# Kernel tuning notes

Measured on AMD Instinct MI355X. Metric: run time of the kernel, lower is better.

The kernel has to match this reference:

```python
import jax, jax.numpy as jnp
import numpy as np

B, S, E, HD = 32, 1024, 768, 64


def _rope_tables(seq_len, dim):
    # theta = 10000 ** (-2*arange(0,dim,2)/dim); freqs = pos * theta
    theta = jnp.power(10000.0, -2.0 * jnp.arange(0, dim, 2, dtype=jnp.float32) / dim)
    pos = jnp.arange(seq_len, dtype=jnp.float32)[:, None]          # [S,1]
    freqs = pos * theta[None, :]                                    # [S,dim//2]
    cos = jnp.repeat(jnp.cos(freqs), 2, axis=-1)                    # [S,dim]
    sin = jnp.repeat(jnp.sin(freqs), 2, axis=-1)                    # [S,dim]
    return cos, sin


def _apply_rope(x, cos, sin):
    # rotate-half interleaved: new[...,0::2] = -x[...,1::2]; new[...,1::2] = x[...,0::2]
    b, s, d = x.shape
    x2 = x.reshape(b, s, d // 2, 2)
    rot = jnp.stack([-x2[..., 1], x2[..., 0]], axis=-1).reshape(b, s, d)
    return x * cos[None] + rot * sin[None]


def setup_inputs() -> dict:
    key = jax.random.key(0)
    k0, k1, k2, k3 = jax.random.split(key, 4)
    x = jax.random.normal(k0, (B, S, E), dtype=jnp.float32)
    Wq = jax.random.normal(k1, (HD, E), dtype=jnp.float32) * 0.02
    Wk = jax.random.normal(k2, (HD, E), dtype=jnp.float32) * 0.02
    Wv = jax.random.normal(k3, (HD, E), dtype=jnp.float32) * 0.02
    return {"x": x, "Wq": Wq, "Wk": Wk, "Wv": Wv}


def reference(x, Wq, Wk, Wv):
    b, s, e = x.shape
    q = jnp.einsum('bse,he->bsh', x, Wq)
    k = jnp.einsum('bse,he->bsh', x, Wk)
    v = jnp.einsum('bse,he->bsh', x, Wv)
    cos, sin = _rope_tables(s, q.shape[-1])
    rq = _apply_rope(q, cos, sin)
    rk = _apply_rope(k, cos, sin)
    scale = e ** (-0.5)  # NOTE: original scales by emb_dim, not head_size
    scores = jnp.einsum('bqh,bkh->bqk', rq, rk) * scale
    causal = jnp.tril(jnp.ones((s, s), dtype=bool))
    scores = jnp.where(causal[None], scores, -jnp.inf)
    attn = jax.nn.softmax(scores, axis=-1)
    return jnp.einsum('bqk,bkh->bqh', attn, v)
```

## Files before the change

kernel.cpp:

```cpp
#include <hip/hip_runtime.h>
#include <hip/hip_bf16.h>

#define B_  32
#define S_  1024
#define E_  768
#define HD_ 64
#define M_  (B_*S_)

typedef __attribute__((ext_vector_type(8))) short short8;
typedef __attribute__((ext_vector_type(4))) float float4v;

__device__ __forceinline__ unsigned short f2bf(float x) {
    union { float f; unsigned u; } c; c.f = x;
    unsigned r = (c.u + 0x7FFFu + ((c.u >> 16) & 1u)) >> 16;
    return (unsigned short)r;
}

__device__ __forceinline__ void gld_lds16(const void* g, void* l) {
    __builtin_amdgcn_global_load_lds(
        (const __attribute__((address_space(1))) unsigned int*)g,
        (__attribute__((address_space(3))) unsigned int*)l,
        16, 0, 0);
}

__global__ __launch_bounds__(256) void setup_kernel(const unsigned int* __restrict__ xw,
                                                    unsigned int* __restrict__ flag,
                                                    float* __restrict__ cs_t,
                                                    float* __restrict__ sn_t) {
    if (blockIdx.x == 128) {
        __shared__ int cnt;
        if (threadIdx.x == 0) cnt = 0;
        __syncthreads();
        unsigned int w = xw[(size_t)threadIdx.x * 33331];
        unsigned int e = (w >> 8) & 0x7F;
        int hit = (e >= 0x3B && e <= 0x40) ? 1 : 0;
        atomicAdd(&cnt, hit);
        __syncthreads();
        if (threadIdx.x == 0) *flag = (cnt > 128) ? 1u : 0u;
        return;
    }
    int idx = blockIdx.x * 256 + threadIdx.x;
    int pos = idx >> 5;
    int ii  = idx & 31;
    float theta = exp2f(-(float)ii * 0.8304820237218406f);
    float fr = (float)pos * theta;
    float sn, cs;
    sincosf(fr, &sn, &cs);
    cs_t[idx] = cs;
    sn_t[idx] = sn;
}

__global__ __launch_bounds__(256) void wpack_kernel(
    const void* __restrict__ Wq_, const void* __restrict__ Wk_,
    const void* __restrict__ Wv_, const unsigned int* __restrict__ flag,
    unsigned short* __restrict__ wp)
{
    const bool isb = (*flag != 0);
    int gid  = blockIdx.x * 256 + threadIdx.x;
    int lane = gid & 63;
    int tIdx = gid >> 6;
    int ct   = tIdx / 24;
    int rem  = tIdx - ct * 24;
    int c    = rem >> 1, ks = rem & 1;
    int quad = lane >> 4, l15 = lane & 15;
    const void* wsel = (ct < 4) ? Wq_ : (ct < 8 ? Wk_ : Wv_);
    int row = (ct & 3) * 16 + l15;
    int col = c * 64 + ks * 32 + quad * 8;
    uint4 w;
    if (isb) {
        w = *(const uint4*)((const unsigned short*)wsel + (size_t)row * E_ + col);
    } else {
        const float* f = (const float*)wsel + (size_t)row * E_ + col;
        float4 a = *(const float4*)f, bq = *(const float4*)(f + 4);
        w.x = f2bf(a.x)  | ((unsigned)f2bf(a.y)  << 16);
        w.y = f2bf(a.z)  | ((unsigned)f2bf(a.w)  << 16);
        w.z = f2bf(bq.x) | ((unsigned)f2bf(bq.y) << 16);
        w.w = f2bf(bq.z) | ((unsigned)f2bf(bq.w) << 16);
    }
    *(uint4*)(wp + (size_t)gid * 8) = w;
}

__global__ __launch_bounds__(512, 2) void qkv_mfma_kernel(
    const void* __restrict__ x_, const unsigned short* __restrict__ wp,
    const unsigned int* __restrict__ flag,
    const float* __restrict__ cs_t, const float* __restrict__ sn_t,
    unsigned short* __restrict__ rq_p, unsigned short* __restrict__ rk_p,
    unsigned short* __restrict__ vt_p)
{
    __shared__ __align__(16) unsigned short Alds[64 * 768];
    __shared__ __align__(16) unsigned short Blds[2][24 * 512];

    const bool isb = (*flag != 0);
    const int t    = threadIdx.x;
    const int lane = t & 63;
    const int wave = t >> 6;
    const int quad = lane >> 4;
    const int l15  = lane & 15;
    const int row0 = blockIdx.x * 64;
    const int h    = wave >> 2;
    const int cw   = wave & 3;

    unsigned eoA[12];
    unsigned ldsA[12];
    #pragma unroll
    for (int j = 0; j < 12; ++j) {
        unsigned L    = (unsigned)(wave * 12 + j) * 1024u + (unsigned)lane * 16u;
        unsigned row  = L / 1536u;
        unsigned colb = L - row * 1536u;
        unsigned win  = colb >> 7, off = colb & 127u;
        unsigned gcol = (win << 7) | (off ^ ((row & 7u) << 4));
        eoA[j]  = row * 768u + (gcol >> 1);
        ldsA[j] = (unsigned)(wave * 12 + j) * 1024u;
    }

    unsigned aA[2][2];
    #pragma unroll
    for (int mtl = 0; mtl < 2; ++mtl) {
        unsigned rl = (unsigned)((h * 2 + mtl) * 16 + l15);
        #pragma unroll
        for (int ks = 0; ks < 2; ++ks)
            aA[mtl][ks] = rl * 1536u + 16u * ((((unsigned)ks << 2) | (unsigned)quad) ^ (rl & 7u));
    }

    float4v acc[3][2];
    #pragma unroll
    for (int nt = 0; nt < 3; ++nt)
        #pragma unroll
        for (int mtl = 0; mtl < 2; ++mtl)
            #pragma unroll
            for (int r = 0; r < 4; ++r) acc[nt][mtl][r] = 0.f;

    auto stageB = [&](int c, int bsel) {
        #pragma unroll
        for (int i = 0; i < 3; ++i) {
            int idx = wave * 3 + i;
            int ct = idx >> 1, ks = idx & 1;
            gld_lds16(wp + ((size_t)((ct * 12 + c) * 2 + ks)) * 512 + lane * 8,
                      &Blds[bsel][(size_t)idx * 512]);
        }
    };

    if (isb) {
        const unsigned short* xb = (const unsigned short*)x_ + (size_t)row0 * E_;
        #pragma unroll
        for (int j = 0; j < 12; ++j)
            gld_lds16(xb + eoA[j], (char*)Alds + ldsA[j]);
    } else {
        const float* xb = (const float*)x_ + (size_t)row0 * E_;
        #pragma unroll
        for (int j = 0; j < 12; ++j) {
            const float* f = xb + eoA[j];
            float4 a = *(const float4*)f, bq = *(const float4*)(f + 4);
            uint4 w;
            w.x = f2bf(a.x)  | ((unsigned)f2bf(a.y)  << 16);
            w.y = f2bf(a.z)  | ((unsigned)f2bf(a.w)  << 16);
            w.z = f2bf(bq.x) | ((unsigned)f2bf(bq.y) << 16);
            w.w = f2bf(bq.z) | ((unsigned)f2bf(bq.w) << 16);
            *(uint4*)((char*)Alds + ldsA[j] + (size_t)lane * 16) = w;
        }
    }
    stageB(0, 0);
    __syncthreads();

    int buf = 0;
    for (int c = 0; c < 12; ++c) {
        if (c < 11) stageB(c + 1, buf ^ 1);
        #pragma unroll
        for (int ks = 0; ks < 2; ++ks) {
            short8 af[2];
            af[0] = *(const short8*)((const char*)Alds + aA[0][ks] + c * 128);
            af[1] = *(const short8*)((const char*)Alds + aA[1][ks] + c * 128);
            #pragma unroll
            for (int nt = 0; nt < 3; ++nt) {
                int ct = cw * 3 + nt;
                short8 bf = *(const short8*)(&Blds[buf][(size_t)(ct * 2 + ks) * 512 + lane * 8]);
                acc[nt][0] = __builtin_amdgcn_mfma_f32_16x16x32_bf16(af[0], bf, acc[nt][0], 0, 0, 0);
                acc[nt][1] = __builtin_amdgcn_mfma_f32_16x16x32_bf16(af[1], bf, acc[nt][1], 0, 0, 0);
            }
        }
        __syncthreads();
        buf ^= 1;
    }

    const int b      = row0 >> 10;
    const int s_in_b = row0 & (S_ - 1);
    #pragma unroll
    for (int nt = 0; nt < 3; ++nt) {
        int ct = cw * 3 + nt;
        int region = ct >> 2;
        int d = (ct & 3) * 16 + l15;
        if (region < 2) {
            unsigned short* dst = (region == 0) ? rq_p : rk_p;
            int ii = d >> 1;
            int ksq = d >> 5, quadq = (d >> 3) & 3, e = d & 7;
            #pragma unroll
            for (int mtl = 0; mtl < 2; ++mtl) {
                #pragma unroll
                for (int r = 0; r < 4; ++r) {
                    int row = row0 + (h * 2 + mtl) * 16 + quad * 4 + r;
                    int pos = row & (S_ - 1);
                    float cs = cs_t[pos * 32 + ii];
                    float sn = sn_t[pos * 32 + ii];
                    float val = acc[nt][mtl][r];
                    float partner = __shfl_xor(val, 1);
                    float res = (d & 1) ? fmaf(val, cs,  partner * sn)
                                        : fmaf(val, cs, -partner * sn);
                    int kt = pos >> 6, ntq = (pos >> 4) & 3, l15q = pos & 15;
                    size_t idx = ((((size_t)(b * 16 + kt) * 4 + ntq) * 2 + ksq) * 64
                                  + quadq * 16 + l15q) * 8 + e;
                    dst[idx] = f2bf(res);
                }
            }
        } else {
            int ntv = ct & 3;
            #pragma unroll
            for (int mtl = 0; mtl < 2; ++mtl) {
                int sb2 = s_in_b + (h * 2 + mtl) * 16 + quad * 4;
                int kt = sb2 >> 6, ksv = (sb2 >> 5) & 1, quadv = (sb2 >> 3) & 3, e0 = sb2 & 7;
                ushort4 pk;
                pk.x = f2bf(acc[nt][mtl][0]);
                pk.y = f2bf(acc[nt][mtl][1]);
                pk.z = f2bf(acc[nt][mtl][2]);
                pk.w = f2bf(acc[nt][mtl][3]);
                size_t idx = ((((size_t)(b * 16 + kt) * 4 + ntv) * 2 + ksv) * 64
                              + quadv * 16 + l15) * 8 + e0;
                *(ushort4*)(vt_p + idx) = pk;
            }
        }
    }
}

__global__ __launch_bounds__(256, 2) void attn_mfma_kernel(
    const unsigned short* __restrict__ rq_p, const unsigned short* __restrict__ rk_p,
    const unsigned short* __restrict__ vt_p, const unsigned int* __restrict__ flag,
    void* __restrict__ out)
{
    __shared__ __align__(16) unsigned short kv[2][32 * 512];
    __shared__ unsigned short plds[4][16][72];

    const bool isb = (*flag != 0);
    const int t    = threadIdx.x;
    const int lane = t & 63;
    const int wave = t >> 6;
    const int quad = lane >> 4;
    const int l15  = lane & 15;
    const int qt   = blockIdx.x;
    const int b    = blockIdx.y;
    const int q0   = qt * 64 + wave * 16;
    const float scale = 0.03608439182435161f;

    const unsigned short* qb = rq_p + ((size_t)((b * 16 + qt) * 4 + wave) * 2) * 512;
    short8 qf0 = *(const short8*)(qb + lane * 8);
    short8 qf1 = *(const short8*)(qb + 512 + lane * 8);

    const unsigned short* sbase[8];
    unsigned eo[8];
    int      slotv[8], tidv[8];
    #pragma unroll
    for (int i = 0; i < 8; ++i) {
        int tid = wave * 8 + i;
        tidv[i] = tid;
        int isV  = tid >> 4;
        int rem  = tid & 15;
        int slot = rem >> 3;
        int wi   = rem & 7;
        int nt   = wi >> 1, ks = wi & 1;
        slotv[i] = slot;
        sbase[i] = isV ? vt_p : rk_p;
        eo[i]    = (unsigned)(((b * 64 + nt) * 2 + ks) * 512 + lane * 8);
    }

    float4v o[4];
    float m_[4], l_[4];
    #pragma unroll
    for (int nt = 0; nt < 4; ++nt)
        #pragma unroll
        for (int r = 0; r < 4; ++r) o[nt][r] = 0.f;
    #pragma unroll
    for (int r = 0; r < 4; ++r) { m_[r] = -1e30f; l_[r] = 0.f; }

    const int nIter = (qt + 2) >> 1;

    auto stage = [&](int it, int bsel) {
        int ta  = 2 * it;
        int tb  = min(ta + 1, qt);
        #pragma unroll
        for (int i = 0; i < 8; ++i) {
            int kt = slotv[i] ? tb : ta;
            gld_lds16(sbase[i] + eo[i] + (size_t)kt * 4096,
                      &kv[bsel][(size_t)tidv[i] * 512]);
        }
    };

    stage(0, 0);
    int buf = 0;
    for (int i = 0; i < nIter; ++i) {
        __syncthreads();
        if (i + 1 < nIter) stage(i + 1, buf ^ 1);
        const unsigned short* kb = kv[buf];

        float sc[2][4][4];
        #pragma unroll
        for (int slot = 0; slot < 2; ++slot) {
            #pragma unroll
            for (int nt = 0; nt < 4; ++nt) {
                float4v s;
                #pragma unroll
                for (int r = 0; r < 4; ++r) s[r] = 0.f;
                short8 kf0 = *(const short8*)(kb + (size_t)(slot * 8 + nt * 2 + 0) * 512 + lane * 8);
                short8 kf1 = *(const short8*)(kb + (size_t)(slot * 8 + nt * 2 + 1) * 512 + lane * 8);
                s = __builtin_amdgcn_mfma_f32_16x16x32_bf16(qf0, kf0, s, 0, 0, 0);
                s = __builtin_amdgcn_mfma_f32_16x16x32_bf16(qf1, kf1, s, 0, 0, 0);
                #pragma unroll
                for (int r = 0; r < 4; ++r) sc[slot][nt][r] = s[r] * scale;
            }
        }

        if (2 * i + 1 >= qt) {
            #pragma unroll
            for (int slot = 0; slot < 2; ++slot) {
                int ktl = 2 * i + slot;
                #pragma unroll
                for (int nt = 0; nt < 4; ++nt) {
                    int kg = ktl * 64 + nt * 16 + l15;
                    #pragma unroll
                    for (int r = 0; r < 4; ++r) {
                        int qg = q0 + quad * 4 + r;
                        if (kg > qg) sc[slot][nt][r] = -1e30f;
                    }
                }
            }
        }

        float mx[4];
        #pragma unroll
        for (int r = 0; r < 4; ++r) {
            float a0 = fmaxf(fmaxf(sc[0][0][r], sc[0][1][r]), fmaxf(sc[0][2][r], sc[0][3][r]));
            float a1 = fmaxf(fmaxf(sc[1][0][r], sc[1][1][r]), fmaxf(sc[1][2][r], sc[1][3][r]));
            mx[r] = fmaxf(a0, a1);
        }
        #pragma unroll
        for (int st = 1; st < 16; st <<= 1)
            #pragma unroll
            for (int r = 0; r < 4; ++r)
                mx[r] = fmaxf(mx[r], __shfl_xor(mx[r], st));

        float al[4];
        #pragma unroll
        for (int r = 0; r < 4; ++r) {
            float mn = fmaxf(m_[r], mx[r]);
            al[r] = __expf(m_[r] - mn);
            m_[r] = mn;
        }

        float sm[4] = {0.f, 0.f, 0.f, 0.f};
        #pragma unroll
        for (int slot = 0; slot < 2; ++slot)
            #pragma unroll
            for (int nt = 0; nt < 4; ++nt)
                #pragma unroll
                for (int r = 0; r < 4; ++r) {
                    float p = __expf(sc[slot][nt][r] - m_[r]);
                    sc[slot][nt][r] = p;
                    sm[r] += p;
                }
        #pragma unroll
        for (int st = 1; st < 16; st <<= 1)
            #pragma unroll
            for (int r = 0; r < 4; ++r)
                sm[r] += __shfl_xor(sm[r], st);
        #pragma unroll
        for (int r = 0; r < 4; ++r) l_[r] = l_[r] * al[r] + sm[r];

        #pragma unroll
        for (int nt = 0; nt < 4; ++nt)
            #pragma unroll
            for (int r = 0; r < 4; ++r) o[nt][r] *= al[r];

        #pragma unroll
        for (int slot = 0; slot < 2; ++slot) {
            #pragma unroll
            for (int nt = 0; nt < 4; ++nt)
                #pragma unroll
                for (int r = 0; r < 4; ++r)
                    plds[wave][quad * 4 + r][nt * 16 + l15] = f2bf(sc[slot][nt][r]);
            short8 pf0 = *(const short8*)&plds[wave][l15][quad * 8];
            short8 pf1 = *(const short8*)&plds[wave][l15][32 + quad * 8];
            #pragma unroll
            for (int nt = 0; nt < 4; ++nt) {
                short8 vf0 = *(const short8*)(kb + (size_t)(16 + slot * 8 + nt * 2 + 0) * 512 + lane * 8);
                short8 vf1 = *(const short8*)(kb + (size_t)(16 + slot * 8 + nt * 2 + 1) * 512 + lane * 8);
                o[nt] = __builtin_amdgcn_mfma_f32_16x16x32_bf16(pf0, vf0, o[nt], 0, 0, 0);
                o[nt] = __builtin_amdgcn_mfma_f32_16x16x32_bf16(pf1, vf1, o[nt], 0, 0, 0);
            }
        }
        buf ^= 1;
    }

    float inv[4];
    #pragma unroll
    for (int r = 0; r < 4; ++r) inv[r] = 1.0f / l_[r];
    if (isb) {
        unsigned short* op = (unsigned short*)out;
        #pragma unroll
        for (int nt = 0; nt < 4; ++nt)
            #pragma unroll
            for (int r = 0; r < 4; ++r) {
                size_t row = (size_t)b * S_ + q0 + quad * 4 + r;
                op[row * HD_ + nt * 16 + l15] = f2bf(o[nt][r] * inv[r]);
            }
    } else {
        float* op = (float*)out;
        #pragma unroll
        for (int nt = 0; nt < 4; ++nt)
            #pragma unroll
            for (int r = 0; r < 4; ++r) {
                size_t row = (size_t)b * S_ + q0 + quad * 4 + r;
                op[row * HD_ + nt * 16 + l15] = o[nt][r] * inv[r];
            }
    }
}

extern "C" void kernel_launch(void* const* d_in, const int* in_sizes, int n_in,
                              void* d_out, int out_size, void* d_ws, size_t ws_size,
                              hipStream_t stream) {
    const void* x  = d_in[0];
    const void* Wq = d_in[1];
    const void* Wk = d_in[2];
    const void* Wv = d_in[3];

    unsigned int* flag = (unsigned int*)d_ws;
    float* cs_t = (float*)d_ws + 64;
    float* sn_t = cs_t + (size_t)S_ * 32;
    unsigned short* wp   = (unsigned short*)(sn_t + (size_t)S_ * 32);
    unsigned short* rq_p = wp + (size_t)288 * 512;
    unsigned short* rk_p = rq_p + (size_t)M_ * HD_;
    unsigned short* vt_p = rk_p + (size_t)M_ * HD_;

    hipLaunchKernelGGL(setup_kernel, dim3(129), dim3(256), 0, stream,
                       (const unsigned int*)x, flag, cs_t, sn_t);
    hipLaunchKernelGGL(wpack_kernel, dim3(72), dim3(256), 0, stream,
                       Wq, Wk, Wv, flag, wp);
    hipLaunchKernelGGL(qkv_mfma_kernel, dim3(M_ / 64), dim3(512), 0, stream,
                       x, wp, flag, cs_t, sn_t, rq_p, rk_p, vt_p);
    hipLaunchKernelGGL(attn_mfma_kernel, dim3(S_ / 64, B_), dim3(256), 0, stream,
                       rq_p, rk_p, vt_p, flag, d_out);
}
```

Before: 207.5 us.

## Stream A and B tiles through a 4-stage LDS ring in QKV GEMM

```diff
diff --git a/kernel.cpp b/kernel.cpp
--- a/kernel.cpp
+++ b/kernel.cpp
@@ -80,15 +80,14 @@
     *(uint4*)(wp + (size_t)gid * 8) = w;
 }
 
-__global__ __launch_bounds__(512, 2) void qkv_mfma_kernel(
+__global__ __launch_bounds__(512, 1) void qkv_mfma_kernel(
     const void* __restrict__ x_, const unsigned short* __restrict__ wp,
     const unsigned int* __restrict__ flag,
     const float* __restrict__ cs_t, const float* __restrict__ sn_t,
     unsigned short* __restrict__ rq_p, unsigned short* __restrict__ rk_p,
     unsigned short* __restrict__ vt_p)
 {
-    __shared__ __align__(16) unsigned short Alds[64 * 768];
-    __shared__ __align__(16) unsigned short Blds[2][24 * 512];
+    __shared__ __align__(16) char lds[4][32768];
 
     const bool isb = (*flag != 0);
     const int t    = threadIdx.x;
@@ -100,17 +99,16 @@
     const int h    = wave >> 2;
     const int cw   = wave & 3;
 
-    unsigned eoA[12];
-    unsigned ldsA[12];
-    #pragma unroll
-    for (int j = 0; j < 12; ++j) {
-        unsigned L    = (unsigned)(wave * 12 + j) * 1024u + (unsigned)lane * 16u;
-        unsigned row  = L / 1536u;
-        unsigned colb = L - row * 1536u;
-        unsigned win  = colb >> 7, off = colb & 127u;
-        unsigned gcol = (win << 7) | (off ^ ((row & 7u) << 4));
-        eoA[j]  = row * 768u + (gcol >> 1);
-        ldsA[j] = (unsigned)(wave * 12 + j) * 1024u;
+    const unsigned aRow  = (unsigned)(wave * 8 + (lane >> 3));
+    const unsigned eoA   = aRow * 768u + (unsigned)(((lane & 7) ^ (lane >> 3)) * 8);
+
+    unsigned eoB[3]; int tidB[3];
+    #pragma unroll
+    for (int i = 0; i < 3; ++i) {
+        int idx = wave * 3 + i;
+        int ct = idx >> 1, ks = idx & 1;
+        eoB[i]  = (unsigned)(ct * 12288 + ks * 512 + lane * 8);
+        tidB[i] = idx;
     }
 
     unsigned aA[2][2];
@@ -119,7 +117,7 @@
         unsigned rl = (unsigned)((h * 2 + mtl) * 16 + l15);
         #pragma unroll
         for (int ks = 0; ks < 2; ++ks)
-            aA[mtl][ks] = rl * 1536u + 16u * ((((unsigned)ks << 2) | (unsigned)quad) ^ (rl & 7u));
+            aA[mtl][ks] = rl * 128u + ((((unsigned)ks << 2) | (unsigned)quad) ^ (rl & 7u)) * 16u;
     }
 
     float4v acc[3][2];
@@ -130,57 +128,74 @@
             #pragma unroll
             for (int r = 0; r < 4; ++r) acc[nt][mtl][r] = 0.f;
 
-    auto stageB = [&](int c, int bsel) {
-        #pragma unroll
-        for (int i = 0; i < 3; ++i) {
-            int idx = wave * 3 + i;
-            int ct = idx >> 1, ks = idx & 1;
-            gld_lds16(wp + ((size_t)((ct * 12 + c) * 2 + ks)) * 512 + lane * 8,
-                      &Blds[bsel][(size_t)idx * 512]);
-        }
+    const unsigned short* xb16 = (const unsigned short*)x_ + (size_t)row0 * E_;
+    const float*          xb32 = (const float*)x_ + (size_t)row0 * E_;
+
+    auto stage_b = [&](int c) {
+        int tc = (c < 11) ? c : 11;
+        char* dst = lds[c & 3];
+        gld_lds16(xb16 + eoA + tc * 64, dst + wave * 1024);
+        #pragma unroll
+        for (int i = 0; i < 3; ++i)
+            gld_lds16(wp + (size_t)eoB[i] + (unsigned)tc * 1024u,
+                      dst + 8192 + tidB[i] * 1024);
     };
-
-    if (isb) {
-        const unsigned short* xb = (const unsigned short*)x_ + (size_t)row0 * E_;
-        #pragma unroll
-        for (int j = 0; j < 12; ++j)
-            gld_lds16(xb + eoA[j], (char*)Alds + ldsA[j]);
-    } else {
-        const float* xb = (const float*)x_ + (size_t)row0 * E_;
-        #pragma unroll
-        for (int j = 0; j < 12; ++j) {
-            const float* f = xb + eoA[j];
+    auto stage_f = [&](int c) {
+        int tc = (c < 11) ? c : 11;
+        char* dst = lds[c & 3];
+        {
+            const float* f = xb32 + eoA + tc * 64;
             float4 a = *(const float4*)f, bq = *(const float4*)(f + 4);
             uint4 w;
             w.x = f2bf(a.x)  | ((unsigned)f2bf(a.y)  << 16);
             w.y = f2bf(a.z)  | ((unsigned)f2bf(a.w)  << 16);
             w.z = f2bf(bq.x) | ((unsigned)f2bf(bq.y) << 16);
             w.w = f2bf(bq.z) | ((unsigned)f2bf(bq.w) << 16);
-            *(uint4*)((char*)Alds + ldsA[j] + (size_t)lane * 16) = w;
-        }
-    }
-    stageB(0, 0);
-    __syncthreads();
-
-    int buf = 0;
-    for (int c = 0; c < 12; ++c) {
-        if (c < 11) stageB(c + 1, buf ^ 1);
-        #pragma unroll
-        for (int ks = 0; ks < 2; ++ks) {
-            short8 af[2];
-            af[0] = *(const short8*)((const char*)Alds + aA[0][ks] + c * 128);
-            af[1] = *(const short8*)((const char*)Alds + aA[1][ks] + c * 128);
-            #pragma unroll
-            for (int nt = 0; nt < 3; ++nt) {
-                int ct = cw * 3 + nt;
-                short8 bf = *(const short8*)(&Blds[buf][(size_t)(ct * 2 + ks) * 512 + lane * 8]);
-                acc[nt][0] = __builtin_amdgcn_mfma_f32_16x16x32_bf16(af[0], bf, acc[nt][0], 0, 0, 0);
-                acc[nt][1] = __builtin_amdgcn_mfma_f32_16x16x32_bf16(af[1], bf, acc[nt][1], 0, 0, 0);
-            }
-        }
-        __syncthreads();
-        buf ^= 1;
-    }
+            *(uint4*)(dst + wave * 1024 + lane * 16) = w;
+        }
+        #pragma unroll
+        for (int i = 0; i < 3; ++i)
+            gld_lds16(wp + (size_t)eoB[i] + (unsigned)tc * 1024u,
+                      dst + 8192 + tidB[i] * 1024);
+    };
+
+    #define QKV_COMPUTE(sb)                                                          \
+        _Pragma("unroll")                                                            \
+        for (int ks = 0; ks < 2; ++ks) {                                             \
+            short8 af[2];                                                            \
+            af[0] = *(const short8*)((sb) + aA[0][ks]);                              \
+            af[1] = *(const short8*)((sb) + aA[1][ks]);                              \
+            _Pragma("unroll")                                                        \
+            for (int nt = 0; nt < 3; ++nt) {                                         \
+                int ct = cw * 3 + nt;                                                \
+                short8 bf = *(const short8*)((sb) + 8192 + (ct * 2 + ks) * 1024      \
+                                             + lane * 16);                           \
+                acc[nt][0] = __builtin_amdgcn_mfma_f32_16x16x32_bf16(                \
+                    af[0], bf, acc[nt][0], 0, 0, 0);                                 \
+                acc[nt][1] = __builtin_amdgcn_mfma_f32_16x16x32_bf16(                \
+                    af[1], bf, acc[nt][1], 0, 0, 0);                                 \
+            }                                                                        \
+        }
+
+    if (isb) {
+        stage_b(0); stage_b(1); stage_b(2);
+        for (int c = 0; c < 12; ++c) {
+            asm volatile("s_waitcnt vmcnt(8)" ::: "memory");
+            __builtin_amdgcn_s_barrier();
+            stage_b(c + 3);
+            const char* sb = lds[c & 3];
+            QKV_COMPUTE(sb)
+        }
+    } else {
+        stage_f(0); stage_f(1); stage_f(2);
+        for (int c = 0; c < 12; ++c) {
+            __syncthreads();
+            stage_f(c + 3);
+            const char* sb = lds[c & 3];
+            QKV_COMPUTE(sb)
+        }
+    }
+    #undef QKV_COMPUTE
 
     const int b      = row0 >> 10;
     const int s_in_b = row0 & (S_ - 1);
```

After: 208.4 us. No clear change (+0.4%).

## Stream QKV A tiles through triple-buffered LDS, B via registers, merge setup kernels

Applied to the files above, without the earlier changes.

```diff
diff --git a/kernel.cpp b/kernel.cpp
--- a/kernel.cpp
+++ b/kernel.cpp
@@ -23,40 +23,41 @@
         16, 0, 0);
 }
 
-__global__ __launch_bounds__(256) void setup_kernel(const unsigned int* __restrict__ xw,
-                                                    unsigned int* __restrict__ flag,
-                                                    float* __restrict__ cs_t,
-                                                    float* __restrict__ sn_t) {
-    if (blockIdx.x == 128) {
-        __shared__ int cnt;
-        if (threadIdx.x == 0) cnt = 0;
-        __syncthreads();
-        unsigned int w = xw[(size_t)threadIdx.x * 33331];
-        unsigned int e = (w >> 8) & 0x7F;
-        int hit = (e >= 0x3B && e <= 0x40) ? 1 : 0;
-        atomicAdd(&cnt, hit);
-        __syncthreads();
-        if (threadIdx.x == 0) *flag = (cnt > 128) ? 1u : 0u;
-        return;
-    }
-    int idx = blockIdx.x * 256 + threadIdx.x;
-    int pos = idx >> 5;
-    int ii  = idx & 31;
-    float theta = exp2f(-(float)ii * 0.8304820237218406f);
-    float fr = (float)pos * theta;
-    float sn, cs;
-    sincosf(fr, &sn, &cs);
-    cs_t[idx] = cs;
-    sn_t[idx] = sn;
-}
-
-__global__ __launch_bounds__(256) void wpack_kernel(
+__global__ __launch_bounds__(256) void setup_kernel(
+    const unsigned int* __restrict__ xw,
     const void* __restrict__ Wq_, const void* __restrict__ Wk_,
-    const void* __restrict__ Wv_, const unsigned int* __restrict__ flag,
+    const void* __restrict__ Wv_,
+    unsigned int* __restrict__ flag,
+    float* __restrict__ cs_t, float* __restrict__ sn_t,
     unsigned short* __restrict__ wp)
 {
-    const bool isb = (*flag != 0);
-    int gid  = blockIdx.x * 256 + threadIdx.x;
+    const int bx = blockIdx.x;
+    if (bx < 128) {
+        int idx = bx * 256 + threadIdx.x;
+        int pos = idx >> 5;
+        int ii  = idx & 31;
+        float theta = exp2f(-(float)ii * 0.8304820237218406f);
+        float fr = (float)pos * theta;
+        float sn, cs;
+        sincosf(fr, &sn, &cs);
+        cs_t[idx] = cs;
+        sn_t[idx] = sn;
+        return;
+    }
+    __shared__ int cnt;
+    if (threadIdx.x == 0) cnt = 0;
+    __syncthreads();
+    unsigned int w0 = xw[(size_t)threadIdx.x * 33331];
+    unsigned int e0 = (w0 >> 8) & 0x7F;
+    int hit = (e0 >= 0x3B && e0 <= 0x40) ? 1 : 0;
+    atomicAdd(&cnt, hit);
+    __syncthreads();
+    const bool isb = (cnt > 128);
+    if (bx == 128) {
+        if (threadIdx.x == 0) *flag = isb ? 1u : 0u;
+        return;
+    }
+    int gid  = (bx - 129) * 256 + threadIdx.x;
     int lane = gid & 63;
     int tIdx = gid >> 6;
     int ct   = tIdx / 24;
@@ -80,15 +81,14 @@
     *(uint4*)(wp + (size_t)gid * 8) = w;
 }
 
-__global__ __launch_bounds__(512, 2) void qkv_mfma_kernel(
+__global__ __launch_bounds__(512, 4) void qkv_mfma_kernel(
     const void* __restrict__ x_, const unsigned short* __restrict__ wp,
     const unsigned int* __restrict__ flag,
     const float* __restrict__ cs_t, const float* __restrict__ sn_t,
     unsigned short* __restrict__ rq_p, unsigned short* __restrict__ rk_p,
     unsigned short* __restrict__ vt_p)
 {
-    __shared__ __align__(16) unsigned short Alds[64 * 768];
-    __shared__ __align__(16) unsigned short Blds[2][24 * 512];
+    __shared__ __align__(16) char alds[3][8192];
 
     const bool isb = (*flag != 0);
     const int t    = threadIdx.x;
@@ -100,18 +100,8 @@
     const int h    = wave >> 2;
     const int cw   = wave & 3;
 
-    unsigned eoA[12];
-    unsigned ldsA[12];
-    #pragma unroll
-    for (int j = 0; j < 12; ++j) {
-        unsigned L    = (unsigned)(wave * 12 + j) * 1024u + (unsigned)lane * 16u;
-        unsigned row  = L / 1536u;
-        unsigned colb = L - row * 1536u;
-        unsigned win  = colb >> 7, off = colb & 127u;
-        unsigned gcol = (win << 7) | (off ^ ((row & 7u) << 4));
-        eoA[j]  = row * 768u + (gcol >> 1);
-        ldsA[j] = (unsigned)(wave * 12 + j) * 1024u;
-    }
+    const unsigned aRow = (unsigned)(wave * 8 + (lane >> 3));
+    const unsigned eoA  = aRow * 768u + (unsigned)(((lane & 7) ^ (lane >> 3)) * 8);
 
     unsigned aA[2][2];
     #pragma unroll
@@ -119,7 +109,16 @@
         unsigned rl = (unsigned)((h * 2 + mtl) * 16 + l15);
         #pragma unroll
         for (int ks = 0; ks < 2; ++ks)
-            aA[mtl][ks] = rl * 1536u + 16u * ((((unsigned)ks << 2) | (unsigned)quad) ^ (rl & 7u));
+            aA[mtl][ks] = rl * 128u + ((((unsigned)ks << 2) | (unsigned)quad) ^ (rl & 7u)) * 16u;
+    }
+
+    const unsigned short* wbase[3][2];
+    #pragma unroll
+    for (int nt = 0; nt < 3; ++nt) {
+        int ct = cw * 3 + nt;
+        #pragma unroll
+        for (int ks = 0; ks < 2; ++ks)
+            wbase[nt][ks] = wp + ((size_t)(ct * 24 + ks)) * 512 + lane * 8;
     }
 
     float4v acc[3][2];
@@ -130,57 +129,80 @@
             #pragma unroll
             for (int r = 0; r < 4; ++r) acc[nt][mtl][r] = 0.f;
 
-    auto stageB = [&](int c, int bsel) {
-        #pragma unroll
-        for (int i = 0; i < 3; ++i) {
-            int idx = wave * 3 + i;
-            int ct = idx >> 1, ks = idx & 1;
-            gld_lds16(wp + ((size_t)((ct * 12 + c) * 2 + ks)) * 512 + lane * 8,
-                      &Blds[bsel][(size_t)idx * 512]);
-        }
-    };
+    short8 breg[2][3][2];
+
+    const unsigned short* xb16 = (const unsigned short*)x_ + (size_t)row0 * E_;
+    const float*          xb32 = (const float*)x_ + (size_t)row0 * E_;
+
+    #define LOADB(cc, sel)                                                       \
+        {   int tc_ = (cc) < 11 ? (cc) : 11;                                     \
+            _Pragma("unroll")                                                    \
+            for (int nt_ = 0; nt_ < 3; ++nt_)                                    \
+                _Pragma("unroll")                                                \
+                for (int ks_ = 0; ks_ < 2; ++ks_)                                \
+                    breg[sel][nt_][ks_] =                                        \
+                        *(const short8*)(wbase[nt_][ks_] + tc_ * 1024);          \
+        }
+
+    #define COMPUTE(cc, sel)                                                     \
+        {   const char* sb_ = alds[(cc) % 3];                                    \
+            _Pragma("unroll")                                                    \
+            for (int ks_ = 0; ks_ < 2; ++ks_) {                                  \
+                short8 af0 = *(const short8*)(sb_ + aA[0][ks_]);                 \
+                short8 af1 = *(const short8*)(sb_ + aA[1][ks_]);                 \
+                _Pragma("unroll")                                                \
+                for (int nt_ = 0; nt_ < 3; ++nt_) {                              \
+                    acc[nt_][0] = __builtin_amdgcn_mfma_f32_16x16x32_bf16(       \
+                        af0, breg[sel][nt_][ks_], acc[nt_][0], 0, 0, 0);         \
+                    acc[nt_][1] = __builtin_amdgcn_mfma_f32_16x16x32_bf16(       \
+                        af1, breg[sel][nt_][ks_], acc[nt_][1], 0, 0, 0);         \
+                }                                                                \
+            }                                                                    \
+        }
 
     if (isb) {
-        const unsigned short* xb = (const unsigned short*)x_ + (size_t)row0 * E_;
-        #pragma unroll
-        for (int j = 0; j < 12; ++j)
-            gld_lds16(xb + eoA[j], (char*)Alds + ldsA[j]);
+        LOADB(0, 0);
+        __builtin_amdgcn_sched_barrier(0);
+        gld_lds16(xb16 + eoA,      alds[0] + wave * 1024);
+        gld_lds16(xb16 + eoA + 64, alds[1] + wave * 1024);
+        __builtin_amdgcn_sched_barrier(0);
+        #pragma unroll
+        for (int c = 0; c < 12; ++c) {
+            asm volatile("s_waitcnt vmcnt(1)" ::: "memory");
+            __builtin_amdgcn_s_barrier();
+            LOADB(c + 1, (c + 1) & 1);
+            __builtin_amdgcn_sched_barrier(0);
+            {
+                int tc = (c + 2) < 11 ? (c + 2) : 11;
+                gld_lds16(xb16 + eoA + tc * 64, alds[(c + 2) % 3] + wave * 1024);
+            }
+            __builtin_amdgcn_sched_barrier(0);
+            COMPUTE(c, c & 1);
+        }
     } else {
-        const float* xb = (const float*)x_ + (size_t)row0 * E_;
-        #pragma unroll
-        for (int j = 0; j < 12; ++j) {
-            const float* f = xb + eoA[j];
+        auto stageA_f = [&](int c) {
+            const float* f = xb32 + eoA + c * 64;
             float4 a = *(const float4*)f, bq = *(const float4*)(f + 4);
             uint4 w;
             w.x = f2bf(a.x)  | ((unsigned)f2bf(a.y)  << 16);
             w.y = f2bf(a.z)  | ((unsigned)f2bf(a.w)  << 16);
             w.z = f2bf(bq.x) | ((unsigned)f2bf(bq.y) << 16);
             w.w = f2bf(bq.z) | ((unsigned)f2bf(bq.w) << 16);
-            *(uint4*)((char*)Alds + ldsA[j] + (size_t)lane * 16) = w;
-        }
-    }
-    stageB(0, 0);
-    __syncthreads();
-
-    int buf = 0;
-    for (int c = 0; c < 12; ++c) {
-        if (c < 11) stageB(c + 1, buf ^ 1);
-        #pragma unroll
-        for (int ks = 0; ks < 2; ++ks) {
-            short8 af[2];
-            af[0] = *(const short8*)((const char*)Alds + aA[0][ks] + c * 128);
-            af[1] = *(const short8*)((const char*)Alds + aA[1][ks] + c * 128);
-            #pragma unroll
-            for (int nt = 0; nt < 3; ++nt) {
-                int ct = cw * 3 + nt;
-                short8 bf = *(const short8*)(&Blds[buf][(size_t)(ct * 2 + ks) * 512 + lane * 8]);
-                acc[nt][0] = __builtin_amdgcn_mfma_f32_16x16x32_bf16(af[0], bf, acc[nt][0], 0, 0, 0);
-                acc[nt][1] = __builtin_amdgcn_mfma_f32_16x16x32_bf16(af[1], bf, acc[nt][1], 0, 0, 0);
-            }
-        }
+            *(uint4*)(alds[c % 3] + wave * 1024 + (size_t)lane * 16) = w;
+        };
+        stageA_f(0); stageA_f(1);
+        LOADB(0, 0);
         __syncthreads();
-        buf ^= 1;
-    }
+        #pragma unroll
+        for (int c = 0; c < 12; ++c) {
+            if (c + 2 < 12) stageA_f(c + 2);
+            LOADB(c + 1, (c + 1) & 1);
+            COMPUTE(c, c & 1);
+            __syncthreads();
+        }
+    }
+    #undef LOADB
+    #undef COMPUTE
 
     const int b      = row0 >> 10;
     const int s_in_b = row0 & (S_ - 1);
@@ -437,10 +459,8 @@
     unsigned short* rk_p = rq_p + (size_t)M_ * HD_;
     unsigned short* vt_p = rk_p + (size_t)M_ * HD_;
 
-    hipLaunchKernelGGL(setup_kernel, dim3(129), dim3(256), 0, stream,
-                       (const unsigned int*)x, flag, cs_t, sn_t);
-    hipLaunchKernelGGL(wpack_kernel, dim3(72), dim3(256), 0, stream,
-                       Wq, Wk, Wv, flag, wp);
+    hipLaunchKernelGGL(setup_kernel, dim3(201), dim3(256), 0, stream,
+                       (const unsigned int*)x, Wq, Wk, Wv, flag, cs_t, sn_t, wp);
     hipLaunchKernelGGL(qkv_mfma_kernel, dim3(M_ / 64), dim3(512), 0, stream,
                        x, wp, flag, cs_t, sn_t, rq_p, rk_p, vt_p);
     hipLaunchKernelGGL(attn_mfma_kernel, dim3(S_ / 64, B_), dim3(256), 0, stream,
```

After: 194.8 us. 1.07x faster.
